# Optimization experiments

Measured on AMD Instinct MI355X. Metric: run time of the kernel, lower is better.

The kernel has to match this reference:

```python
import jax, jax.numpy as jnp
import numpy as np
from jax import lax

N = 50000      # nodes
E = 1600000    # edges
F = 128        # input features
G = 32         # gnn_hidden_dim
H = 50         # lstm hidden_dim
SEQ = 10       # sequence_length


def setup_inputs() -> dict:
    key = jax.random.key(0)
    ks = jax.random.split(key, 12)
    s = 0.05
    return {
        "x": jax.random.normal(ks[0], (N, F), jnp.float32),
        "W_gcn": jax.random.normal(ks[1], (F, G), jnp.float32) * s,
        "b_gcn": jnp.zeros((G,), jnp.float32),
        "w_ih0": jax.random.normal(ks[2], (4 * H, G), jnp.float32) * s,
        "w_hh0": jax.random.normal(ks[3], (4 * H, H), jnp.float32) * s,
        "b_ih0": jnp.zeros((4 * H,), jnp.float32),
        "b_hh0": jnp.zeros((4 * H,), jnp.float32),
        "w_ih1": jax.random.normal(ks[4], (4 * H, H), jnp.float32) * s,
        "w_hh1": jax.random.normal(ks[5], (4 * H, H), jnp.float32) * s,
        "b_ih1": jnp.zeros((4 * H,), jnp.float32),
        "b_hh1": jnp.zeros((4 * H,), jnp.float32),
        "fc_w": jax.random.normal(ks[6], (1, H), jnp.float32) * s,
        "fc_b": jnp.zeros((1,), jnp.float32),
        "edge_index": jax.random.randint(ks[7], (2, E), 0, N, dtype=jnp.int64),
        "seq_len": SEQ,
    }


def gcn_conv(x, edge_index, W, b):
    # PyG GCNConv: add self-loops, symmetric deg^{-1/2} normalization,
    # linear transform, gather-scale-scatter aggregation at target nodes.
    n = x.shape[0]
    loop = jnp.arange(n, dtype=edge_index.dtype)
    src = jnp.concatenate([edge_index[0], loop])  # message sources j
    dst = jnp.concatenate([edge_index[1], loop])  # aggregation targets i
    deg = jax.ops.segment_sum(jnp.ones_like(dst, dtype=x.dtype), dst,
                              num_segments=n)
    dinv = jnp.where(deg > 0, lax.rsqrt(jnp.maximum(deg, 1.0)), 0.0)
    norm = dinv[src] * dinv[dst]                       # [E+N]
    h = x @ W                                          # [N, G]
    msg = h[src] * norm[:, None]                       # gather + scale
    out = jax.ops.segment_sum(msg, dst, num_segments=n)
    return out + b


def lstm_layer(x_proj, w_hh, b_hh):
    # x_proj: [T, B, 4H] precomputed input projections (i,f,g,o gate order).
    T, B, H4 = x_proj.shape
    Hd = H4 // 4
    h0 = jnp.zeros((B, Hd), x_proj.dtype)
    c0 = jnp.zeros((B, Hd), x_proj.dtype)

    def step(carry, xp):
        h, c = carry
        gates = xp + h @ w_hh.T + b_hh
        i, f, g, o = jnp.split(gates, 4, axis=-1)
        i, f, o = jax.nn.sigmoid(i), jax.nn.sigmoid(f), jax.nn.sigmoid(o)
        g = jnp.tanh(g)
        c = f * c + i * g
        h = o * jnp.tanh(c)
        return (h, c), h

    (h, c), ys = lax.scan(step, (h0, c0), x_proj)
    return ys, h


def reference(x, W_gcn, b_gcn, w_ih0, w_hh0, b_ih0, b_hh0,
              w_ih1, w_hh1, b_ih1, b_hh1, fc_w, fc_b,
              edge_index, seq_len):
    gnn_out = gcn_conv(x, edge_index, W_gcn, b_gcn)        # [N, G]
    # lstm_in = gnn_out repeated seq_len times -> input projection is
    # identical per step; compute once and broadcast (same math).
    p0 = gnn_out @ w_ih0.T + b_ih0                         # [N, 4H]
    x_proj0 = jnp.broadcast_to(p0, (seq_len,) + p0.shape)  # [T, N, 4H]
    ys0, _ = lstm_layer(x_proj0, w_hh0, b_hh0)             # [T, N, H]
    x_proj1 = ys0 @ w_ih1.T + b_ih1                        # [T, N, 4H]
    _, hn1 = lstm_layer(x_proj1, w_hh1, b_hh1)             # [N, H]
    return hn1 @ fc_w.T + fc_b                             # [N, 1]
```

## Files before the change

### kernel.cpp

```cpp
#include <hip/hip_runtime.h>
#include <hip/hip_bf16.h>

typedef __attribute__((ext_vector_type(8))) short short8;
typedef __attribute__((ext_vector_type(4))) float f32x4;

#define L2E 1.442695041f
#define SCAN_B 256

__device__ __forceinline__ short f2bf(float f) {
  union { __hip_bfloat16 b; short s; } u;
  u.b = __float2bfloat16(f);
  return u.s;
}
__device__ __forceinline__ float b2f(short s) {
  unsigned u = ((unsigned)(unsigned short)s) << 16;
  return __uint_as_float(u);
}

__device__ __forceinline__ float ldh(const float* p, size_t i) { return p[i]; }
__device__ __forceinline__ float ldh(const __hip_bfloat16* p, size_t i) {
  return __bfloat162float(p[i]);
}
__device__ __forceinline__ void sth(float* p, size_t i, float v) { p[i] = v; }
__device__ __forceinline__ void sth(__hip_bfloat16* p, size_t i, float v) {
  p[i] = __float2bfloat16(v);
}

__device__ __forceinline__ short8 load_gfrag(const float* g, size_t base) {
  const float4* gp = (const float4*)(g + base);
  float4 a = gp[0], b = gp[1];
  short8 t;
  t[0]=f2bf(a.x); t[1]=f2bf(a.y); t[2]=f2bf(a.z); t[3]=f2bf(a.w);
  t[4]=f2bf(b.x); t[5]=f2bf(b.y); t[6]=f2bf(b.z); t[7]=f2bf(b.w);
  return t;
}
__device__ __forceinline__ short8 load_gfrag(const __hip_bfloat16* g, size_t base) {
  return *(const short8*)(g + base);
}

#define OFF_WIH0 0
#define OFF_WHH0 13312
#define OFF_WIH1 39936
#define OFF_WHH1 66560
#define OFF_B0   93184
#define OFF_B1   94016
#define OFF_FCW  94848
#define IMG_BYTES 95104

__global__ void k_detect(const int* __restrict__ ei, int E, int* __restrict__ flag) {
  if (threadIdx.x == 0 && blockIdx.x == 0) {
    int odd_nz = 0, even_nz = 0;
    int m = min(128, E);
    for (int i = 0; i < m; ++i) {
      odd_nz |= (ei[2 * i + 1] != 0);
      even_nz |= (ei[2 * i] != 0);
    }
    *flag = (even_nz && !odd_nz) ? 1 : 0;
  }
}


__global__ void k_count(const int* __restrict__ ei, int E,
                        const int* __restrict__ flag, int* __restrict__ cnt) {
  int e = blockIdx.x * blockDim.x + threadIdx.x;
  if (e < E) {
    int d = (*flag) ? ei[2 * (E + e)] : ei[E + e];
    atomicAdd(&cnt[d], 1);
  }
}

__global__ void k_convert(const int* __restrict__ ei, int E,
                          unsigned int* __restrict__ ed, int* __restrict__ cnt) {
  __shared__ int sflag;
  if (threadIdx.x == 0) {
    int odd_nz = 0, even_nz = 0;
    int m = min(128, E);
    for (int i = 0; i < m; ++i) {
      odd_nz |= (ei[2 * i + 1] != 0);
      even_nz |= (ei[2 * i] != 0);
    }
    sflag = (even_nz && !odd_nz) ? 1 : 0;
  }
  __syncthreads();
  int is64 = sflag;
  int e = blockIdx.x * blockDim.x + threadIdx.x;
  if (e < E) {
    int s = is64 ? ei[2 * e] : ei[e];
    int d = is64 ? ei[2 * (E + e)] : ei[E + e];
    ed[e] = (unsigned int)s | ((unsigned int)d << 16);
    atomicAdd(&cnt[d], 1);
  }
}

__global__ void k_dinv(const int* __restrict__ cnt, float* __restrict__ dinv, int N) {
  int i = blockIdx.x * blockDim.x + threadIdx.x;
  if (i < N) dinv[i] = rsqrtf((float)cnt[i] + 1.0f);
}

__global__ __launch_bounds__(256) void k_scanA(const int* __restrict__ cnt,
                                               float* __restrict__ dinv,
                                               int* __restrict__ bsum, int N) {
  __shared__ int red[256];
  int b = blockIdx.x, t = threadIdx.x;
  int chunk = (N + SCAN_B - 1) / SCAN_B;
  int lo = b * chunk, hi = min(lo + chunk, N);
  int s = 0;
  for (int i = lo + t; i < hi; i += 256) {
    int c = cnt[i];
    dinv[i] = rsqrtf((float)c + 1.0f);
    s += c;
  }
  red[t] = s;
  __syncthreads();
  for (int o = 128; o > 0; o >>= 1) {
    if (t < o) red[t] += red[t + o];
    __syncthreads();
  }
  if (t == 0) bsum[b] = red[0];
}

__global__ __launch_bounds__(256) void k_scanB(int* __restrict__ a,
                                               const int* __restrict__ bsum,
                                               int N) {
  __shared__ int sh[256];
  int b = blockIdx.x, t = threadIdx.x;
  int chunk = (N + SCAN_B - 1) / SCAN_B;
  int lo = b * chunk, hi = min(lo + chunk, N);
  sh[t] = bsum[t];
  __syncthreads();
  for (int o = 1; o < 256; o <<= 1) {
    int u = (t >= o) ? sh[t - o] : 0;
    __syncthreads();
    sh[t] += u;
    __syncthreads();
  }
  int carry = (b == 0) ? 0 : sh[b - 1];
  __syncthreads();
  for (int i0 = lo; i0 < hi; i0 += 256) {
    int i = i0 + t;
    int c = (i < hi) ? a[i] : 0;
    sh[t] = c;
    __syncthreads();
    for (int o = 1; o < 256; o <<= 1) {
      int u = (t >= o) ? sh[t - o] : 0;
      __syncthreads();
      sh[t] += u;
      __syncthreads();
    }
    if (i < hi) a[i] = carry + sh[t] - c;
    carry += sh[255];
    __syncthreads();
  }
}

__global__ void k_fill_p(const unsigned int* __restrict__ ed, int E,
                         int* __restrict__ rowst,
                         unsigned short* __restrict__ csr, int lo, int hi) {
  int e = blockIdx.x * blockDim.x + threadIdx.x;
  if (e < E) {
    unsigned int v = ed[e];
    int d = (int)(v >> 16);
    if (d >= lo && d < hi) {
      int p = atomicAdd(&rowst[d], 1);
      csr[p] = (unsigned short)(v & 0xFFFFu);
    }
  }
}

template <typename CT>
__global__ void k_fill(const int* __restrict__ ei, int E,
                       const int* __restrict__ flag,
                       int* __restrict__ rowst, CT* __restrict__ csr,
                       int lo, int hi) {
  int e = blockIdx.x * blockDim.x + threadIdx.x;
  if (e < E) {
    int is64 = *flag;
    int d = is64 ? ei[2 * (E + e)] : ei[E + e];
    if (d >= lo && d < hi) {
      int s = is64 ? ei[2 * e] : ei[e];
      int p = atomicAdd(&rowst[d], 1);
      csr[p] = (CT)s;
    }
  }
}

template <typename HT>
__global__ __launch_bounds__(256) void k_hs(const float* __restrict__ x,
                                            const float* __restrict__ Wg,
                                            const float* __restrict__ dinv,
                                            HT* __restrict__ hs, int N) {
  __shared__ __align__(16) float xt[64][132];
  __shared__ __align__(16) float Wl[128][32];
  int tid = threadIdx.x;
  int nb = blockIdx.x * 64;
  for (int i = tid; i < 4096; i += 256) Wl[i >> 5][i & 31] = Wg[i];
  const float4* xv = (const float4*)x;
  for (int i = tid; i < 2048; i += 256) {
    int r = i >> 5, c = i & 31;
    float4 v = make_float4(0.f, 0.f, 0.f, 0.f);
    if (nb + r < N) v = xv[(size_t)(nb + r) * 32 + c];
    *(float4*)&xt[r][c * 4] = v;
  }
  __syncthreads();
  int nl = tid >> 2, gq = (tid & 3) * 8;
  float a[8];
#pragma unroll
  for (int j = 0; j < 8; ++j) a[j] = 0.f;
  for (int k = 0; k < 128; ++k) {
    float xk = xt[nl][k];
#pragma unroll
    for (int j = 0; j < 8; ++j) a[j] += xk * Wl[k][gq + j];
  }
  int n = nb + nl;
  if (n < N) {
    float d = dinv[n];
#pragma unroll
    for (int j = 0; j < 8; ++j) sth(hs, (size_t)n * 32 + gq + j, a[j] * d);
  }
}

template <typename HT, typename GT, typename CT>
__global__ void k_gather4(const CT* __restrict__ csr, const int* __restrict__ rowst,
                          const HT* __restrict__ hs, const float* __restrict__ dinv,
                          const float* __restrict__ bg, GT* __restrict__ gout,
                          int N) {
  long long gtid = (long long)blockIdx.x * blockDim.x + threadIdx.x;
  int wave = (int)(gtid >> 6);
  int n0 = wave * 4;
  if (n0 >= N) return;
  int l = threadIdx.x & 63;
  int gf = l & 31, j = l >> 5;
  int rr = 0;
  int ri = n0 - 1 + l;
  if (l <= 4 && ri >= 0 && ri < N) rr = rowst[ri];
  int st[4], en[4], idx[4], deg[4];
#pragma unroll
  for (int q = 0; q < 4; ++q) {
    st[q] = __shfl(rr, q);
    en[q] = __shfl(rr, q + 1);
    deg[q] = en[q] - st[q];
  }
#pragma unroll
  for (int q = 0; q < 4; ++q)
    idx[q] = (n0 + q < N && l < deg[q]) ? (int)csr[st[q] + l] : 0;
  float bgv = bg[gf];
#pragma unroll
  for (int q = 0; q < 4; ++q) {
    int w = n0 + q;
    if (w >= N) break;
    float acc = 0.f;
    int dm = min(deg[q], 64);
#pragma unroll 1
    for (int base = 0; base < 64; base += 16) {
      if (base >= dm) break;
#pragma unroll
      for (int i = 0; i < 8; ++i) {
        int e = base + 2 * i + j;
        int src = __shfl(idx[q], e);
        float v = ldh(hs, (size_t)src * 32 + gf);
        acc += (e < dm) ? v : 0.f;
      }
    }
    for (int k2 = st[q] + 64 + j; k2 < en[q]; k2 += 2)
      acc += ldh(hs, (size_t)csr[k2] * 32 + gf);
    acc += __shfl_xor(acc, 32);
    if (j == 0) {
      float v = (acc + ldh(hs, (size_t)w * 32 + gf)) * dinv[w] + bgv;
      sth(gout, (size_t)w * 32 + gf, v);
    }
  }
}

template <typename HT>
__global__ void k_scatter(const int* __restrict__ ei, int E,
                          const int* __restrict__ flag,
                          const HT* __restrict__ hs, float* __restrict__ gout) {
  long long gid = (long long)blockIdx.x * blockDim.x + threadIdx.x;
  int e = (int)(gid >> 3), part = (int)(gid & 7);
  if (e >= E) return;
  int is64 = *flag;
  int s = is64 ? ei[2 * e] : ei[e];
  int d = is64 ? ei[2 * (E + e)] : ei[E + e];
  int b = part * 4;
  float* gp = gout + (size_t)d * 32 + b;
  size_t hp = (size_t)s * 32 + b;
  atomicAdd(gp + 0, ldh(hs, hp + 0));
  atomicAdd(gp + 1, ldh(hs, hp + 1));
  atomicAdd(gp + 2, ldh(hs, hp + 2));
  atomicAdd(gp + 3, ldh(hs, hp + 3));
}
template <typename HT>
__global__ void k_finish(const HT* __restrict__ hs, const float* __restrict__ dinv,
                         const float* __restrict__ bg, float* __restrict__ gout,
                         int N) {
  int gid = blockIdx.x * blockDim.x + threadIdx.x;
  if (gid < N * 32) {
    int n = gid >> 5, g = gid & 31;
    gout[gid] = (gout[gid] + ldh(hs, (size_t)gid)) * dinv[n] + bg[g];
  }
}

__global__ void k_prep(const float* __restrict__ wih0, const float* __restrict__ whh0,
                       const float* __restrict__ wih1, const float* __restrict__ whh1,
                       const float* __restrict__ bih0, const float* __restrict__ bhh0,
                       const float* __restrict__ bih1, const float* __restrict__ bhh1,
                       const float* __restrict__ fcw, unsigned char* __restrict__ img,
                       int* __restrict__ rowst, int N) {
  int gid = blockIdx.x * blockDim.x + threadIdx.x;
  int nthr = gridDim.x * blockDim.x;
  for (int i = gid; i < N; i += nthr) rowst[i] = 0;
  {
    short* W = (short*)(img + OFF_WIH0);
    for (int i = gid; i < 208 * 32; i += nthr) {
      int row = i >> 5, k = i & 31, u = row >> 2, q = row & 3;
      float sc = (q == 2) ? 2.0f * L2E : -L2E;
      float v = (u < 50) ? wih0[(q * 50 + u) * 32 + k] * sc : 0.0f;
      W[row * 32 + (k ^ ((row & 3) << 3))] = f2bf(v);
    }
  }
  {
    short* W = (short*)(img + OFF_WHH0);
    for (int i = gid; i < 208 * 64; i += nthr) {
      int row = i >> 6, k = i & 63, u = row >> 2, q = row & 3;
      float sc = (q == 2) ? 2.0f * L2E : -L2E;
      float v = (u < 50 && k < 50) ? whh0[(q * 50 + u) * 50 + k] * sc : 0.0f;
      W[row * 64 + (k ^ ((row & 7) << 3))] = f2bf(v);
    }
  }
  {
    short* W = (short*)(img + OFF_WIH1);
    for (int i = gid; i < 208 * 64; i += nthr) {
      int row = i >> 6, k = i & 63, u = row >> 2, q = row & 3;
      float sc = (q == 2) ? 2.0f * L2E : -L2E;
      float v = (u < 50 && k < 50) ? wih1[(q * 50 + u) * 50 + k] * sc : 0.0f;
      W[row * 64 + (k ^ ((row & 7) << 3))] = f2bf(v);
    }
  }
  {
    short* W = (short*)(img + OFF_WHH1);
    for (int i = gid; i < 208 * 64; i += nthr) {
      int row = i >> 6, k = i & 63, u = row >> 2, q = row & 3;
      float sc = (q == 2) ? 2.0f * L2E : -L2E;
      float v = (u < 50 && k < 50) ? whh1[(q * 50 + u) * 50 + k] * sc : 0.0f;
      W[row * 64 + (k ^ ((row & 7) << 3))] = f2bf(v);
    }
  }
  {
    float* B = (float*)(img + OFF_B0);
    for (int i = gid; i < 208; i += nthr) {
      int u = i >> 2, q = i & 3;
      float sc = (q == 2) ? 2.0f * L2E : -L2E;
      B[i] = (u < 50) ? (bih0[q * 50 + u] + bhh0[q * 50 + u]) * sc : 0.0f;
    }
  }
  {
    float* B = (float*)(img + OFF_B1);
    for (int i = gid; i < 208; i += nthr) {
      int u = i >> 2, q = i & 3;
      float sc = (q == 2) ? 2.0f * L2E : -L2E;
      B[i] = (u < 50) ? (bih1[q * 50 + u] + bhh1[q * 50 + u]) * sc : 0.0f;
    }
  }
  {
    float* F = (float*)(img + OFF_FCW);
    for (int i = gid; i < 64; i += nthr) F[i] = (i < 50) ? fcw[i] : 0.0f;
  }
}

__device__ __forceinline__ float gate_update(const f32x4& acc, float& cp) {
  float ei = __builtin_amdgcn_exp2f(acc[0]);
  float ef = __builtin_amdgcn_exp2f(acc[1]);
  float eo = __builtin_amdgcn_exp2f(acc[3]);
  float eg = __builtin_amdgcn_exp2f(fminf(acc[2], 80.0f));
  float a = 1.0f + ei, b = 1.0f + ef;
  float rif = __builtin_amdgcn_rcpf(a * b);
  float iv = rif * b, fv = rif * a;
  float o1 = 1.0f + eo, g1 = eg + 1.0f;
  float rog = __builtin_amdgcn_rcpf(o1 * g1);
  float ov = rog * g1;
  float gv = (eg - 1.0f) * (rog * o1);
  float c = fv * cp + iv * gv;
  cp = c;
  float Ec = __builtin_amdgcn_exp2f(c * (2.0f * L2E));
  float th = (Ec - 1.0f) * __builtin_amdgcn_rcpf(Ec + 1.0f);
  return ov * th;
}

template <typename GT>
__global__ __launch_bounds__(512, 2) void k_lstm(const GT* __restrict__ gout,
    const unsigned char* __restrict__ img, const float* __restrict__ fcb_p,
    float* __restrict__ out, int N) {
  __shared__ __align__(16) unsigned char smem[160640];
  const int tid = threadIdx.x;
  {
    const uint4* s = (const uint4*)img;
    uint4* d = (uint4*)smem;
    for (int i = tid; i < IMG_BYTES / 16; i += 512) d[i] = s[i];
  }
  __syncthreads();
  const int lane = tid & 63, wid = tid >> 6;
  const int l15 = lane & 15, l4 = lane >> 4;
  const int swz7 = (l15 & 7) << 3, swz3 = (l15 & 3) << 3;
  const int node0 = blockIdx.x * 256 + wid * 32;

  const short* WIH0 = (const short*)(smem + OFF_WIH0);
  const short* WHH0 = (const short*)(smem + OFF_WHH0);
  const short* WIH1 = (const short*)(smem + OFF_WIH1);
  const short* WHH1 = (const short*)(smem + OFF_WHH1);
  const float* B0   = (const float*)(smem + OFF_B0);
  const float* B1   = (const float*)(smem + OFF_B1);
  const float* FCW  = (const float*)(smem + OFF_FCW);
  short* h0st = (short*)(smem + IMG_BYTES + wid * 8192);
  short* h1st = h0st + 2048;

  {
    uint4 z; z.x = z.y = z.z = z.w = 0u;
    uint4* p = (uint4*)h0st;
    for (int i = lane; i < 512; i += 64) p[i] = z;
  }

  f32x4 p0r[13][2];
  {
    short8 gfrag[2];
#pragma unroll
    for (int v = 0; v < 2; ++v) {
      int node = node0 + v * 16 + l15;
      short8 t = {0, 0, 0, 0, 0, 0, 0, 0};
      if (node < N) t = load_gfrag(gout, (size_t)node * 32 + l4 * 8);
      gfrag[v] = t;
    }
#pragma unroll
    for (int t = 0; t < 13; ++t) {
      short8 w = *(const short8*)(WIH0 + (16 * t + l15) * 32 + ((l4 * 8) ^ swz3));
      f32x4 bv = *(const f32x4*)(B0 + t * 16 + l4 * 4);
#pragma unroll
      for (int v = 0; v < 2; ++v)
        p0r[t][v] = __builtin_amdgcn_mfma_f32_16x16x32_bf16(w, gfrag[v], bv, 0, 0, 0);
    }
  }

  float c0[13][2], c1[13][2];
#pragma unroll
  for (int t = 0; t < 13; ++t) { c0[t][0]=0.f; c0[t][1]=0.f; c1[t][0]=0.f; c1[t][1]=0.f; }

#pragma unroll 1
  for (int s = 0; s < 10; ++s) {
    short8 h0f[2][2], h1f[2][2];
#pragma unroll
    for (int c = 0; c < 2; ++c)
#pragma unroll
      for (int v = 0; v < 2; ++v) {
        int nl = v * 16 + l15;
        h0f[c][v] = *(const short8*)(h0st + nl * 64 + ((c * 32 + l4 * 8) ^ swz7));
        h1f[c][v] = *(const short8*)(h1st + nl * 64 + ((c * 32 + l4 * 8) ^ swz7));
      }
#pragma unroll
    for (int t = 0; t < 13; ++t) {
      int arow = (16 * t + l15);
      short8 ah0 = *(const short8*)(WHH0 + arow * 64 + ((l4 * 8) ^ swz7));
      short8 ah1 = *(const short8*)(WHH0 + arow * 64 + ((32 + l4 * 8) ^ swz7));
#pragma unroll
      for (int v = 0; v < 2; ++v) {
        f32x4 acc = p0r[t][v];
        acc = __builtin_amdgcn_mfma_f32_16x16x32_bf16(ah0, h0f[0][v], acc, 0, 0, 0);
        acc = __builtin_amdgcn_mfma_f32_16x16x32_bf16(ah1, h0f[1][v], acc, 0, 0, 0);
        float h = gate_update(acc, c0[t][v]);
        h0st[(v * 16 + l15) * 64 + ((4 * t + l4) ^ swz7)] = f2bf(h);
      }
    }
    short8 h0nf[2][2];
#pragma unroll
    for (int c = 0; c < 2; ++c)
#pragma unroll
      for (int v = 0; v < 2; ++v) {
        int nl = v * 16 + l15;
        h0nf[c][v] = *(const short8*)(h0st + nl * 64 + ((c * 32 + l4 * 8) ^ swz7));
      }
#pragma unroll
    for (int t = 0; t < 13; ++t) {
      f32x4 bv = *(const f32x4*)(B1 + t * 16 + l4 * 4);
      int arow = (16 * t + l15);
      short8 ai0 = *(const short8*)(WIH1 + arow * 64 + ((l4 * 8) ^ swz7));
      short8 ai1 = *(const short8*)(WIH1 + arow * 64 + ((32 + l4 * 8) ^ swz7));
      short8 ah0 = *(const short8*)(WHH1 + arow * 64 + ((l4 * 8) ^ swz7));
      short8 ah1 = *(const short8*)(WHH1 + arow * 64 + ((32 + l4 * 8) ^ swz7));
#pragma unroll
      for (int v = 0; v < 2; ++v) {
        f32x4 acc = bv;
        acc = __builtin_amdgcn_mfma_f32_16x16x32_bf16(ai0, h0nf[0][v], acc, 0, 0, 0);
        acc = __builtin_amdgcn_mfma_f32_16x16x32_bf16(ai1, h0nf[1][v], acc, 0, 0, 0);
        acc = __builtin_amdgcn_mfma_f32_16x16x32_bf16(ah0, h1f[0][v], acc, 0, 0, 0);
        acc = __builtin_amdgcn_mfma_f32_16x16x32_bf16(ah1, h1f[1][v], acc, 0, 0, 0);
        float h = gate_update(acc, c1[t][v]);
        h1st[(v * 16 + l15) * 64 + ((4 * t + l4) ^ swz7)] = f2bf(h);
      }
    }
  }
  float fcb = fcb_p[0];
#pragma unroll
  for (int v = 0; v < 2; ++v) {
    int nl = v * 16 + l15;
    float facc = 0.f;
#pragma unroll
    for (int c = 0; c < 2; ++c) {
      short8 f = *(const short8*)(h1st + nl * 64 + ((c * 32 + l4 * 8) ^ swz7));
#pragma unroll
      for (int j = 0; j < 8; ++j)
        facc += b2f(f[j]) * FCW[c * 32 + l4 * 8 + j];
    }
    facc += __shfl_xor(facc, 16);
    facc += __shfl_xor(facc, 32);
    int node = node0 + v * 16 + l15;
    if (l4 == 0 && node < N) out[node] = facc + fcb;
  }
}

extern "C" void kernel_launch(void* const* d_in, const int* in_sizes, int n_in,
                              void* d_out, int out_size, void* d_ws, size_t ws_size,
                              hipStream_t stream) {
  const float* x    = (const float*)d_in[0];
  const float* Wg   = (const float*)d_in[1];
  const float* bg   = (const float*)d_in[2];
  const float* wih0 = (const float*)d_in[3];
  const float* whh0 = (const float*)d_in[4];
  const float* bih0 = (const float*)d_in[5];
  const float* bhh0 = (const float*)d_in[6];
  const float* wih1 = (const float*)d_in[7];
  const float* whh1 = (const float*)d_in[8];
  const float* bih1 = (const float*)d_in[9];
  const float* bhh1 = (const float*)d_in[10];
  const float* fcw  = (const float*)d_in[11];
  const float* fcb  = (const float*)d_in[12];
  const int*   edge = (const int*)d_in[13];
  int N = in_sizes[0] / 128;
  int E = in_sizes[13] / 2;

  char* ws = (char*)d_ws;
  size_t off = 0;
  auto take = [&](size_t b) {
    size_t o = off;
    off = (off + b + 255) & ~(size_t)255;
    return o;
  };
  int*   rowst = (int*)(ws + take((size_t)N * 4));
  float* dinv  = (float*)(ws + take((size_t)N * 4));
  int*   flag  = (int*)(ws + take(256));
  unsigned char* wimg = (unsigned char*)(ws + take(IMG_BYTES));
  size_t base = off;

  const int NP = 4;
  int span = (N + NP - 1) / NP;
  bool canU16 = (N <= 65535) && (E <= 100000000);

  size_t csr_b  = ((size_t)E * 2 + 255) & ~(size_t)255;
  size_t hsb    = ((size_t)N * 64 + 255) & ~(size_t)255;
  size_t reg2_b = (size_t)E * 4 > 2 * hsb ? (size_t)E * 4 : 2 * hsb;
  size_t needP  = base + csr_b + reg2_b;
  size_t needA = base + (((size_t)N * 128 + 255) & ~(size_t)255)
               + (((size_t)E * 4 + 255) & ~(size_t)255)
               + ((size_t)N * 128);

  k_prep<<<52, 256, 0, stream>>>(wih0, whh0, wih1, whh1, bih0, bhh0, bih1, bhh1,
                                 fcw, wimg, rowst, N);

  if (canU16 && ws_size >= needP) {
    unsigned short* csr = (unsigned short*)(ws + take(csr_b));
    char* reg2 = ws + take(reg2_b);
    unsigned int*   ed   = (unsigned int*)reg2;
    __hip_bfloat16* hs   = (__hip_bfloat16*)reg2;
    __hip_bfloat16* gout = (__hip_bfloat16*)(reg2 + hsb);
    int* bsum = (int*)csr;

    k_convert<<<(E + 255) / 256, 256, 0, stream>>>(edge, E, ed, rowst);
    k_scanA<<<SCAN_B, 256, 0, stream>>>(rowst, dinv, bsum, N);
    k_scanB<<<SCAN_B, 256, 0, stream>>>(rowst, bsum, N);
    for (int p = 0; p < NP; ++p) {
      int lo = p * span, hi = min(lo + span, N);
      if (lo >= hi) break;
      k_fill_p<<<(E + 255) / 256, 256, 0, stream>>>(ed, E, rowst, csr, lo, hi);
    }
    k_hs<__hip_bfloat16><<<(N + 63) / 64, 256, 0, stream>>>(x, Wg, dinv, hs, N);
    int gwaves = (N + 3) / 4;
    k_gather4<__hip_bfloat16, __hip_bfloat16, unsigned short>
        <<<(gwaves * 64 + 255) / 256, 256, 0, stream>>>(csr, rowst, hs, dinv,
                                                        bg, gout, N);
    k_lstm<__hip_bfloat16><<<(N + 255) / 256, 512, 0, stream>>>(gout, wimg, fcb,
                                                                (float*)d_out, N);
  } else if (ws_size >= needA) {
    float* gout = (float*)(ws + take((size_t)N * 128));
    int*   csr  = (int*)(ws + take((size_t)E * 4));
    float* hs   = (float*)(ws + take((size_t)N * 128));
    int*   bsum = (int*)csr;
    k_detect<<<1, 1, 0, stream>>>(edge, E, flag);
    k_count<<<(E + 255) / 256, 256, 0, stream>>>(edge, E, flag, rowst);
    k_scanA<<<SCAN_B, 256, 0, stream>>>(rowst, dinv, bsum, N);
    k_scanB<<<SCAN_B, 256, 0, stream>>>(rowst, bsum, N);
    k_hs<float><<<(N + 63) / 64, 256, 0, stream>>>(x, Wg, dinv, hs, N);
    for (int p = 0; p < NP; ++p) {
      int lo = p * span, hi = min(lo + span, N);
      if (lo >= hi) break;
      k_fill<int><<<(E + 255) / 256, 256, 0, stream>>>(edge, E, flag, rowst,
                                                       csr, lo, hi);
    }
    int gwaves = (N + 3) / 4;
    k_gather4<float, float, int><<<(gwaves * 64 + 255) / 256, 256, 0, stream>>>(
        csr, rowst, hs, dinv, bg, gout, N);
    k_lstm<float><<<(N + 255) / 256, 512, 0, stream>>>(gout, wimg, fcb,
                                                       (float*)d_out, N);
  } else {
    float* gout = (float*)(ws + take((size_t)N * 128));
    __hip_bfloat16* hs = (__hip_bfloat16*)(ws + take((size_t)N * 64));
    hipMemsetAsync(gout, 0, (size_t)N * 128, stream);
    k_detect<<<1, 1, 0, stream>>>(edge, E, flag);
    k_count<<<(E + 255) / 256, 256, 0, stream>>>(edge, E, flag, rowst);
    k_dinv<<<(N + 255) / 256, 256, 0, stream>>>(rowst, dinv, N);
    k_hs<__hip_bfloat16><<<(N + 63) / 64, 256, 0, stream>>>(x, Wg, dinv, hs, N);
    int sc_blocks = (int)(((long long)E * 8 + 255) / 256);
    k_scatter<__hip_bfloat16><<<sc_blocks, 256, 0, stream>>>(edge, E, flag, hs, gout);
    k_finish<__hip_bfloat16><<<(N * 32 + 255) / 256, 256, 0, stream>>>(
        hs, dinv, bg, gout, N);
    k_lstm<float><<<(N + 255) / 256, 512, 0, stream>>>(gout, wimg, fcb,
                                                       (float*)d_out, N);
  }
}
```

Baseline: 323.1 us.

## Split LSTM work to 16 nodes per wave with 1024-thread blocks

```diff
diff --git a/kernel.cpp b/kernel.cpp
--- a/kernel.cpp
+++ b/kernel.cpp
@@ -387,7 +387,7 @@
 }
 
 template <typename GT>
-__global__ __launch_bounds__(512, 2) void k_lstm(const GT* __restrict__ gout,
+__global__ __launch_bounds__(1024, 1) void k_lstm(const GT* __restrict__ gout,
     const unsigned char* __restrict__ img, const float* __restrict__ fcb_p,
     float* __restrict__ out, int N) {
   __shared__ __align__(16) unsigned char smem[160640];
@@ -395,13 +395,13 @@
   {
     const uint4* s = (const uint4*)img;
     uint4* d = (uint4*)smem;
-    for (int i = tid; i < IMG_BYTES / 16; i += 512) d[i] = s[i];
+    for (int i = tid; i < IMG_BYTES / 16; i += 1024) d[i] = s[i];
   }
   __syncthreads();
   const int lane = tid & 63, wid = tid >> 6;
   const int l15 = lane & 15, l4 = lane >> 4;
   const int swz7 = (l15 & 7) << 3, swz3 = (l15 & 3) << 3;
-  const int node0 = blockIdx.x * 256 + wid * 32;
+  const int node0 = blockIdx.x * 256 + wid * 16;
 
   const short* WIH0 = (const short*)(smem + OFF_WIH0);
   const short* WHH0 = (const short*)(smem + OFF_WHH0);
@@ -410,72 +410,55 @@
   const float* B0   = (const float*)(smem + OFF_B0);
   const float* B1   = (const float*)(smem + OFF_B1);
   const float* FCW  = (const float*)(smem + OFF_FCW);
-  short* h0st = (short*)(smem + IMG_BYTES + wid * 8192);
-  short* h1st = h0st + 2048;
+  short* h0st = (short*)(smem + IMG_BYTES + wid * 4096);
+  short* h1st = h0st + 1024;
 
   {
     uint4 z; z.x = z.y = z.z = z.w = 0u;
     uint4* p = (uint4*)h0st;
-    for (int i = lane; i < 512; i += 64) p[i] = z;
-  }
-
-  f32x4 p0r[13][2];
-  {
-    short8 gfrag[2];
-#pragma unroll
-    for (int v = 0; v < 2; ++v) {
-      int node = node0 + v * 16 + l15;
-      short8 t = {0, 0, 0, 0, 0, 0, 0, 0};
-      if (node < N) t = load_gfrag(gout, (size_t)node * 32 + l4 * 8);
-      gfrag[v] = t;
-    }
+    for (int i = lane; i < 256; i += 64) p[i] = z;
+  }
+
+  f32x4 p0r[13];
+  {
+    short8 gfrag = {0, 0, 0, 0, 0, 0, 0, 0};
+    int node = node0 + l15;
+    if (node < N) gfrag = load_gfrag(gout, (size_t)node * 32 + l4 * 8);
 #pragma unroll
     for (int t = 0; t < 13; ++t) {
       short8 w = *(const short8*)(WIH0 + (16 * t + l15) * 32 + ((l4 * 8) ^ swz3));
       f32x4 bv = *(const f32x4*)(B0 + t * 16 + l4 * 4);
-#pragma unroll
-      for (int v = 0; v < 2; ++v)
-        p0r[t][v] = __builtin_amdgcn_mfma_f32_16x16x32_bf16(w, gfrag[v], bv, 0, 0, 0);
-    }
-  }
-
-  float c0[13][2], c1[13][2];
-#pragma unroll
-  for (int t = 0; t < 13; ++t) { c0[t][0]=0.f; c0[t][1]=0.f; c1[t][0]=0.f; c1[t][1]=0.f; }
+      p0r[t] = __builtin_amdgcn_mfma_f32_16x16x32_bf16(w, gfrag, bv, 0, 0, 0);
+    }
+  }
+
+  float c0[13], c1[13];
+#pragma unroll
+  for (int t = 0; t < 13; ++t) { c0[t] = 0.f; c1[t] = 0.f; }
 
 #pragma unroll 1
   for (int s = 0; s < 10; ++s) {
-    short8 h0f[2][2], h1f[2][2];
+    short8 h0f[2];
 #pragma unroll
     for (int c = 0; c < 2; ++c)
-#pragma unroll
-      for (int v = 0; v < 2; ++v) {
-        int nl = v * 16 + l15;
-        h0f[c][v] = *(const short8*)(h0st + nl * 64 + ((c * 32 + l4 * 8) ^ swz7));
-        h1f[c][v] = *(const short8*)(h1st + nl * 64 + ((c * 32 + l4 * 8) ^ swz7));
-      }
+      h0f[c] = *(const short8*)(h0st + l15 * 64 + ((c * 32 + l4 * 8) ^ swz7));
 #pragma unroll
     for (int t = 0; t < 13; ++t) {
       int arow = (16 * t + l15);
       short8 ah0 = *(const short8*)(WHH0 + arow * 64 + ((l4 * 8) ^ swz7));
       short8 ah1 = *(const short8*)(WHH0 + arow * 64 + ((32 + l4 * 8) ^ swz7));
-#pragma unroll
-      for (int v = 0; v < 2; ++v) {
-        f32x4 acc = p0r[t][v];
-        acc = __builtin_amdgcn_mfma_f32_16x16x32_bf16(ah0, h0f[0][v], acc, 0, 0, 0);
-        acc = __builtin_amdgcn_mfma_f32_16x16x32_bf16(ah1, h0f[1][v], acc, 0, 0, 0);
-        float h = gate_update(acc, c0[t][v]);
-        h0st[(v * 16 + l15) * 64 + ((4 * t + l4) ^ swz7)] = f2bf(h);
-      }
-    }
-    short8 h0nf[2][2];
-#pragma unroll
-    for (int c = 0; c < 2; ++c)
-#pragma unroll
-      for (int v = 0; v < 2; ++v) {
-        int nl = v * 16 + l15;
-        h0nf[c][v] = *(const short8*)(h0st + nl * 64 + ((c * 32 + l4 * 8) ^ swz7));
-      }
+      f32x4 acc = p0r[t];
+      acc = __builtin_amdgcn_mfma_f32_16x16x32_bf16(ah0, h0f[0], acc, 0, 0, 0);
+      acc = __builtin_amdgcn_mfma_f32_16x16x32_bf16(ah1, h0f[1], acc, 0, 0, 0);
+      float h = gate_update(acc, c0[t]);
+      h0st[l15 * 64 + ((4 * t + l4) ^ swz7)] = f2bf(h);
+    }
+    short8 h0nf[2], h1f[2];
+#pragma unroll
+    for (int c = 0; c < 2; ++c) {
+      h0nf[c] = *(const short8*)(h0st + l15 * 64 + ((c * 32 + l4 * 8) ^ swz7));
+      h1f[c]  = *(const short8*)(h1st + l15 * 64 + ((c * 32 + l4 * 8) ^ swz7));
+    }
 #pragma unroll
     for (int t = 0; t < 13; ++t) {
       f32x4 bv = *(const f32x4*)(B1 + t * 16 + l4 * 4);
@@ -484,35 +467,28 @@
       short8 ai1 = *(const short8*)(WIH1 + arow * 64 + ((32 + l4 * 8) ^ swz7));
       short8 ah0 = *(const short8*)(WHH1 + arow * 64 + ((l4 * 8) ^ swz7));
       short8 ah1 = *(const short8*)(WHH1 + arow * 64 + ((32 + l4 * 8) ^ swz7));
-#pragma unroll
-      for (int v = 0; v < 2; ++v) {
-        f32x4 acc = bv;
-        acc = __builtin_amdgcn_mfma_f32_16x16x32_bf16(ai0, h0nf[0][v], acc, 0, 0, 0);
-        acc = __builtin_amdgcn_mfma_f32_16x16x32_bf16(ai1, h0nf[1][v], acc, 0, 0, 0);
-        acc = __builtin_amdgcn_mfma_f32_16x16x32_bf16(ah0, h1f[0][v], acc, 0, 0, 0);
-        acc = __builtin_amdgcn_mfma_f32_16x16x32_bf16(ah1, h1f[1][v], acc, 0, 0, 0);
-        float h = gate_update(acc, c1[t][v]);
-        h1st[(v * 16 + l15) * 64 + ((4 * t + l4) ^ swz7)] = f2bf(h);
-      }
+      f32x4 acc = bv;
+      acc = __builtin_amdgcn_mfma_f32_16x16x32_bf16(ai0, h0nf[0], acc, 0, 0, 0);
+      acc = __builtin_amdgcn_mfma_f32_16x16x32_bf16(ai1, h0nf[1], acc, 0, 0, 0);
+      acc = __builtin_amdgcn_mfma_f32_16x16x32_bf16(ah0, h1f[0], acc, 0, 0, 0);
+      acc = __builtin_amdgcn_mfma_f32_16x16x32_bf16(ah1, h1f[1], acc, 0, 0, 0);
+      float h = gate_update(acc, c1[t]);
+      h1st[l15 * 64 + ((4 * t + l4) ^ swz7)] = f2bf(h);
     }
   }
   float fcb = fcb_p[0];
-#pragma unroll
-  for (int v = 0; v < 2; ++v) {
-    int nl = v * 16 + l15;
-    float facc = 0.f;
-#pragma unroll
-    for (int c = 0; c < 2; ++c) {
-      short8 f = *(const short8*)(h1st + nl * 64 + ((c * 32 + l4 * 8) ^ swz7));
-#pragma unroll
-      for (int j = 0; j < 8; ++j)
-        facc += b2f(f[j]) * FCW[c * 32 + l4 * 8 + j];
-    }
-    facc += __shfl_xor(facc, 16);
-    facc += __shfl_xor(facc, 32);
-    int node = node0 + v * 16 + l15;
-    if (l4 == 0 && node < N) out[node] = facc + fcb;
-  }
+  float facc = 0.f;
+#pragma unroll
+  for (int c = 0; c < 2; ++c) {
+    short8 f = *(const short8*)(h1st + l15 * 64 + ((c * 32 + l4 * 8) ^ swz7));
+#pragma unroll
+    for (int j = 0; j < 8; ++j)
+      facc += b2f(f[j]) * FCW[c * 32 + l4 * 8 + j];
+  }
+  facc += __shfl_xor(facc, 16);
+  facc += __shfl_xor(facc, 32);
+  int node = node0 + l15;
+  if (l4 == 0 && node < N) out[node] = facc + fcb;
 }
 
 extern "C" void kernel_launch(void* const* d_in, const int* in_sizes, int n_in,
@@ -584,8 +560,8 @@
     k_gather4<__hip_bfloat16, __hip_bfloat16, unsigned short>
         <<<(gwaves * 64 + 255) / 256, 256, 0, stream>>>(csr, rowst, hs, dinv,
                                                         bg, gout, N);
-    k_lstm<__hip_bfloat16><<<(N + 255) / 256, 512, 0, stream>>>(gout, wimg, fcb,
-                                                                (float*)d_out, N);
+    k_lstm<__hip_bfloat16><<<(N + 255) / 256, 1024, 0, stream>>>(gout, wimg, fcb,
+                                                                 (float*)d_out, N);
   } else if (ws_size >= needA) {
     float* gout = (float*)(ws + take((size_t)N * 128));
     int*   csr  = (int*)(ws + take((size_t)E * 4));
@@ -605,8 +581,8 @@
     int gwaves = (N + 3) / 4;
     k_gather4<float, float, int><<<(gwaves * 64 + 255) / 256, 256, 0, stream>>>(
         csr, rowst, hs, dinv, bg, gout, N);
-    k_lstm<float><<<(N + 255) / 256, 512, 0, stream>>>(gout, wimg, fcb,
-                                                       (float*)d_out, N);
+    k_lstm<float><<<(N + 255) / 256, 1024, 0, stream>>>(gout, wimg, fcb,
+                                                        (float*)d_out, N);
   } else {
     float* gout = (float*)(ws + take((size_t)N * 128));
     __hip_bfloat16* hs = (__hip_bfloat16*)(ws + take((size_t)N * 64));
@@ -619,7 +595,7 @@
     k_scatter<__hip_bfloat16><<<sc_blocks, 256, 0, stream>>>(edge, E, flag, hs, gout);
     k_finish<__hip_bfloat16><<<(N * 32 + 255) / 256, 256, 0, stream>>>(
         hs, dinv, bg, gout, N);
-    k_lstm<float><<<(N + 255) / 256, 512, 0, stream>>>(gout, wimg, fcb,
-                                                       (float*)d_out, N);
-  }
-}
+    k_lstm<float><<<(N + 255) / 256, 1024, 0, stream>>>(gout, wimg, fcb,
+                                                        (float*)d_out, N);
+  }
+}
```

Measured after the change: 327.8 us. About the same (+1.5%).
